# Kernel optimization log

Hardware: AMD Instinct MI355X
Metric: run time of the kernel (lower is better)

## Reference

```python
import jax, jax.numpy as jnp
import numpy as np

ALPHA = 0.2  # LeakyReLU negative slope
NEG_BIG = jnp.float32(-9e15)


def _leaky_relu(x):
    return jnp.where(x > 0, x, ALPHA * x)


def gat_layer(h, adj, w, a):
    """One GATLayer with concat=True (ELU output), dropout=0 (eval mode).
    h: [N, F_in], adj: [N, N] int, w: [F_in, F_out], a: [2*F_out, 1].
    """
    Wh = h @ w                         # [N, F_out]
    f_out = w.shape[1]
    Wh1 = Wh @ a[:f_out]               # [N, 1]
    Wh2 = Wh @ a[f_out:]               # [N, 1]
    e = _leaky_relu(Wh1 + Wh2.T)       # [N, N] dense additive scores
    att = jnp.where(adj > 0, e, NEG_BIG)
    att = jax.nn.softmax(att, axis=1)  # row softmax
    return jax.nn.elu(att @ Wh)        # [N, F_out]


def setup_inputs() -> dict:
    N, F_IN, H, NHEADS = 4096, 128, 64, 4
    key = jax.random.key(0)
    ks = jax.random.split(key, 9)
    s = jnp.float32(0.1)  # keep logits in a sane range
    x = jax.random.normal(ks[0], (N, F_IN), jnp.float32)
    adj = jax.random.randint(ks[1], (N, N), 0, 2, jnp.int32)
    return {
        "x": x,
        "adj": adj,
        "w_heads": jax.random.normal(ks[2], (NHEADS, F_IN, H), jnp.float32) * s,
        "a_heads": jax.random.normal(ks[3], (NHEADS, 2 * H, 1), jnp.float32) * s,
        "w_out": jax.random.normal(ks[4], (NHEADS * H, H), jnp.float32) * s,
        "a_out": jax.random.normal(ks[5], (2 * H, 1), jnp.float32) * s,
        "lin_w": jax.random.normal(ks[6], (H, F_IN), jnp.float32) * s,
        "lin_b": jnp.zeros((H,), jnp.float32),
        "outlin_w": jax.random.normal(ks[7], (H, H), jnp.float32) * s,
        "outlin_b": jnp.zeros((H,), jnp.float32),
    }


def reference(x, adj, w_heads, a_heads, w_out, a_out, lin_w, lin_b, outlin_w, outlin_b):
    N = x.shape[0]
    x_residual = x @ lin_w.T + lin_b                      # nn.Linear(input, hidden)
    # multi-head GAT layers, concatenated along features
    heads = jax.vmap(gat_layer, in_axes=(None, None, 0, 0))(x, adj, w_heads, a_heads)  # [nh, N, H]
    hcat = jnp.transpose(heads, (1, 0, 2)).reshape(N, -1)  # [N, nh*H]
    out = gat_layer(hcat, adj, w_out, a_out)               # out_att (concat=True => ELU)
    out = (x_residual + out) @ outlin_w.T + outlin_b       # out_linear
    return jax.nn.elu(out)
```

## Files before the change

kernel.cpp:

```cpp
#include <hip/hip_runtime.h>
#include <hip/hip_bf16.h>
#include <stdint.h>

#define F_IN 128
#define H 64
#define NH 4
#define KCH_H 8
#define KCH_O 16
#define LOG2E 1.44269504088896f

typedef __attribute__((ext_vector_type(8))) short bf16x8;
typedef __attribute__((ext_vector_type(4))) float floatx4;

static __device__ __forceinline__ unsigned short f2bf(float v) {
    __hip_bfloat16 b = __float2bfloat16(v);
    return *(unsigned short*)&b;
}

__global__ void prep_kernel(const int4* __restrict__ adj4,
                            unsigned char* __restrict__ adjp,
                            const float* __restrict__ x,
                            const float* __restrict__ w_heads,
                            const float* __restrict__ a_heads,
                            const float* __restrict__ lin_w,
                            const float* __restrict__ lin_b,
                            unsigned short* __restrict__ Bpk,
                            float* __restrict__ x_res,
                            float* __restrict__ s1h,
                            float* __restrict__ s2h, int N) {
    int bid = blockIdx.x;
    int tid = threadIdx.x;
    int KT = N >> 5;
    if (bid < 2 * N) {
        int row = bid >> 1;
        int c0 = ((bid & 1) * 256 + tid) * 8;
        const int4* p = adj4 + ((size_t)row * N + c0) / 4;
        int4 a = p[0], b = p[1];
        unsigned int byte =
            (unsigned)(a.x > 0) | ((unsigned)(a.y > 0) << 1) |
            ((unsigned)(a.z > 0) << 2) | ((unsigned)(a.w > 0) << 3) |
            ((unsigned)(b.x > 0) << 4) | ((unsigned)(b.y > 0) << 5) |
            ((unsigned)(b.z > 0) << 6) | ((unsigned)(b.w > 0) << 7);
        int kt = c0 >> 5, q = (c0 >> 3) & 3;
        adjp[((size_t)(row >> 4) * KT + kt) * 64 + q * 16 + (row & 15)] =
            (unsigned char)byte;
        return;
    }
    int blk = bid - 2 * N;
    int h = tid >> 6, f = tid & 63;
    int i0 = blk * 8;
    __shared__ float xs[8][F_IN];
    for (int e = tid; e < 8 * F_IN; e += 256)
        xs[e >> 7][e & 127] = x[(size_t)(i0 + (e >> 7)) * F_IN + (e & 127)];
    __syncthreads();
    float acc[8];
#pragma unroll
    for (int r = 0; r < 8; ++r) acc[r] = 0.f;
    float xr0 = 0.f, xr1 = 0.f;
    const float* w = w_heads + (size_t)h * F_IN * H + f;
    const float* lw = lin_w + (size_t)f * F_IN;
#pragma unroll 4
    for (int k = 0; k < F_IN; ++k) {
        float wv = w[(size_t)k * H];
#pragma unroll
        for (int r = 0; r < 8; ++r) acc[r] += xs[r][k] * wv;
        float wx = lw[k];
        xr0 += xs[h][k] * wx;
        xr1 += xs[h + 4][k] * wx;
    }
    {
        int kt = i0 >> 5, qq = (i0 >> 3) & 3;
        union { unsigned short s[8]; uint4 v; } t;
#pragma unroll
        for (int r = 0; r < 8; ++r) t.s[r] = f2bf(acc[r]);
        unsigned short* d = Bpk +
            (((size_t)(h * KT + kt) * 4 + (f >> 4)) * 64 + qq * 16 + (f & 15)) * 8;
        *(uint4*)d = t.v;
    }
    float b = lin_b[f];
    x_res[(size_t)(i0 + h) * H + f] = xr0 + b;
    x_res[(size_t)(i0 + h + 4) * H + f] = xr1 + b;
    float a1v = a_heads[(size_t)h * 2 * H + f];
    float a2v = a_heads[(size_t)h * 2 * H + H + f];
#pragma unroll
    for (int r = 0; r < 8; ++r) {
        float t1 = acc[r] * a1v;
        float t2 = acc[r] * a2v;
#pragma unroll
        for (int off = 32; off > 0; off >>= 1) {
            t1 += __shfl_xor(t1, off, 64);
            t2 += __shfl_xor(t2, off, 64);
        }
        if (f == 0) {
            s1h[(size_t)h * N + i0 + r] = t1 * LOG2E;
            s2h[(size_t)h * N + i0 + r] = t2 * LOG2E;
        }
    }
}

template <int KTC>
__global__ __launch_bounds__(256, 8)
void pv2_kernel(const unsigned char* __restrict__ adjp,
                const unsigned short* __restrict__ Bpk,
                const float* __restrict__ s1a,
                const float* __restrict__ s2a,
                float* __restrict__ outp, float* __restrict__ lp,
                int out_stride, int N) {
    const int h = blockIdx.y, z = blockIdx.z;
    const int KT = N >> 5;
    const int kt0 = z * KTC;
    const int tid = threadIdx.x;
    const int wave = tid >> 6, lane = tid & 63;
    const int n = lane & 15, q = lane >> 4;
    const int i0w = (blockIdx.x * 4 + wave) * 16;

    __shared__ float s2s[KTC * 32];
    __shared__ unsigned short ldsB[2][2048];

    const float4* s2src = (const float4*)(s2a + (size_t)h * N + kt0 * 32);
    for (int e = tid; e < KTC * 8; e += 256) ((float4*)s2s)[e] = s2src[e];

    const unsigned short* Bb = Bpk + ((size_t)h * KT + kt0) * 2048;
    uint4 breg = *(const uint4*)(Bb + tid * 8);
    *(uint4*)&ldsB[0][tid * 8] = breg;
    breg = *(const uint4*)(Bb + 2048 + tid * 8);

    const unsigned char* ap = adjp + ((size_t)(i0w >> 4) * KT + kt0) * 64 + lane;
    unsigned int a_c = ap[0];
    unsigned int a_n = ap[64];
    const float s1v = s1a[(size_t)h * N + i0w + n];

    floatx4 acc[4];
    floatx4 accl = {0.f, 0.f, 0.f, 0.f};
#pragma unroll
    for (int g = 0; g < 4; ++g) acc[g] = (floatx4){0.f, 0.f, 0.f, 0.f};

    bf16x8 ones;
    {
        short one = (n == 0) ? (short)0x3F80 : (short)0;
#pragma unroll
        for (int jj = 0; jj < 8; ++jj) ones[jj] = one;
    }

    __syncthreads();

#pragma unroll 2
    for (int k = 0; k < KTC; ++k) {
        if (k + 1 < KTC) *(uint4*)&ldsB[(k + 1) & 1][tid * 8] = breg;
        unsigned int a_2 = 0;
        if (k + 2 < KTC) {
            breg = *(const uint4*)(Bb + (size_t)(k + 2) * 2048 + tid * 8);
            a_2 = ap[(size_t)(k + 2) * 64];
        }

        float4 sa = *(const float4*)&s2s[k * 32 + q * 8];
        float4 sb = *(const float4*)&s2s[k * 32 + q * 8 + 4];
        const float* sv = (const float*)&sa;
        const float* sw = (const float*)&sb;
        float e[8];
#pragma unroll
        for (int jj = 0; jj < 8; ++jj) {
            float sj = (jj < 4 ? sv[jj] : sw[jj - 4]);
            float tt = s1v + sj;
            float lr = fmaxf(tt, 0.2f * tt);
            lr = (a_c & (1u << jj)) ? lr : -150.f;
            e[jj] = __builtin_amdgcn_exp2f(lr);
        }
        union { unsigned int u[4]; bf16x8 v; } u;
        u.u[0] = __builtin_amdgcn_perm(__float_as_uint(e[1]), __float_as_uint(e[0]), 0x07060302u);
        u.u[1] = __builtin_amdgcn_perm(__float_as_uint(e[3]), __float_as_uint(e[2]), 0x07060302u);
        u.u[2] = __builtin_amdgcn_perm(__float_as_uint(e[5]), __float_as_uint(e[4]), 0x07060302u);
        u.u[3] = __builtin_amdgcn_perm(__float_as_uint(e[7]), __float_as_uint(e[6]), 0x07060302u);

        bf16x8 bf0 = *(const bf16x8*)&ldsB[k & 1][0 * 512 + lane * 8];
        bf16x8 bf1 = *(const bf16x8*)&ldsB[k & 1][1 * 512 + lane * 8];
        bf16x8 bf2 = *(const bf16x8*)&ldsB[k & 1][2 * 512 + lane * 8];
        bf16x8 bf3 = *(const bf16x8*)&ldsB[k & 1][3 * 512 + lane * 8];

        acc[0] = __builtin_amdgcn_mfma_f32_16x16x32_bf16(u.v, bf0, acc[0], 0, 0, 0);
        acc[1] = __builtin_amdgcn_mfma_f32_16x16x32_bf16(u.v, bf1, acc[1], 0, 0, 0);
        acc[2] = __builtin_amdgcn_mfma_f32_16x16x32_bf16(u.v, bf2, acc[2], 0, 0, 0);
        acc[3] = __builtin_amdgcn_mfma_f32_16x16x32_bf16(u.v, bf3, acc[3], 0, 0, 0);
        accl   = __builtin_amdgcn_mfma_f32_16x16x32_bf16(u.v, ones, accl, 0, 0, 0);

        a_c = a_n;
        a_n = a_2;
        __syncthreads();
    }

    float* obase = outp + ((size_t)z * N + i0w) * out_stride + h * 64;
#pragma unroll
    for (int r = 0; r < 4; ++r) {
        int rr = q * 4 + r;
        float* op = obase + (size_t)rr * out_stride + n;
        op[0]  = acc[0][r];
        op[16] = acc[1][r];
        op[32] = acc[2][r];
        op[48] = acc[3][r];
    }
    if (n == 0) {
        float* lrow = lp + ((size_t)z * gridDim.y + h) * N + i0w;
#pragma unroll
        for (int r = 0; r < 4; ++r) lrow[q * 4 + r] = accl[r];
    }
}

__global__ void whout2_kernel(const float* __restrict__ hcp,
                              const float* __restrict__ lhp,
                              const float* __restrict__ w_out,
                              const float* __restrict__ a_out,
                              unsigned short* __restrict__ BpkO,
                              float* __restrict__ s1o,
                              float* __restrict__ s2o, int N) {
    int tid = threadIdx.x;
    int i0 = blockIdx.x * 8;
    int KT = N >> 5;
    __shared__ float hs[8][256];
    __shared__ float linv[8][NH];
    if (tid < 8 * NH) {
        int r = tid >> 2, hd = tid & 3;
        float l = 0.f;
#pragma unroll
        for (int p = 0; p < KCH_H; ++p)
            l += lhp[((size_t)p * NH + hd) * N + i0 + r];
        linv[r][hd] = 1.f / fmaxf(l, 1e-30f);
    }
    __syncthreads();
    const size_t ps = (size_t)N * 256;
    for (int e = tid; e < 8 * 256; e += 256) {
        int r = e >> 8, k = e & 255;
        size_t off = (size_t)(i0 + r) * 256 + k;
        float v = 0.f;
#pragma unroll
        for (int p = 0; p < KCH_H; ++p) v += hcp[p * ps + off];
        v *= linv[r][k >> 6];
        hs[r][k] = v > 0.f ? v : expm1f(v);
    }
    __syncthreads();
    int f = tid & 63, rl = tid >> 6;
    float a0 = 0.f, a1 = 0.f;
#pragma unroll 4
    for (int k = 0; k < 256; ++k) {
        float wv = w_out[(size_t)k * H + f];
        a0 += hs[rl][k] * wv;
        a1 += hs[rl + 4][k] * wv;
    }
    float w1 = a_out[f], w2 = a_out[H + f];
    float t10 = a0 * w1, t20 = a0 * w2, t11 = a1 * w1, t21 = a1 * w2;
#pragma unroll
    for (int off = 32; off > 0; off >>= 1) {
        t10 += __shfl_xor(t10, off, 64);
        t20 += __shfl_xor(t20, off, 64);
        t11 += __shfl_xor(t11, off, 64);
        t21 += __shfl_xor(t21, off, 64);
    }
    if (f == 0) {
        s1o[i0 + rl] = t10 * LOG2E;
        s2o[i0 + rl] = t20 * LOG2E;
        s1o[i0 + rl + 4] = t11 * LOG2E;
        s2o[i0 + rl + 4] = t21 * LOG2E;
    }
    __syncthreads();
    float* wsW = &hs[0][0];
    wsW[rl * 64 + f] = a0;
    wsW[(rl + 4) * 64 + f] = a1;
    __syncthreads();
    if (tid < 64) {
        int kt = i0 >> 5, qq = (i0 >> 3) & 3;
        int g = tid >> 4, nn = tid & 15;
        union { unsigned short s[8]; uint4 v; } t;
#pragma unroll
        for (int r = 0; r < 8; ++r) t.s[r] = f2bf(wsW[r * 64 + g * 16 + nn]);
        unsigned short* d = BpkO +
            (((size_t)kt * 4 + g) * 64 + qq * 16 + nn) * 8;
        *(uint4*)d = t.v;
    }
}

__global__ void final2_kernel(const float* __restrict__ o2p,
                              const float* __restrict__ lop,
                              const float* __restrict__ x_res,
                              const float* __restrict__ outlin_w,
                              const float* __restrict__ outlin_b,
                              float* __restrict__ out, int N) {
    int tid = threadIdx.x;
    int f = tid & 63, rl = tid >> 6;
    int i0 = blockIdx.x * 8;
    __shared__ float hs[8][H];
    __shared__ float linv[8];
    if (tid < 8) {
        float l = 0.f;
#pragma unroll
        for (int p = 0; p < KCH_O; ++p) l += lop[(size_t)p * N + i0 + tid];
        linv[tid] = 1.f / fmaxf(l, 1e-30f);
    }
    __syncthreads();
    const size_t ps = (size_t)N * 64;
    for (int e = tid; e < 8 * 64; e += 256) {
        int r = e >> 6, ff = e & 63;
        size_t off = (size_t)(i0 + r) * 64 + ff;
        float v = 0.f;
#pragma unroll
        for (int p = 0; p < KCH_O; ++p) v += o2p[p * ps + off];
        v *= linv[r];
        v = v > 0.f ? v : expm1f(v);
        hs[r][ff] = v + x_res[off];
    }
    __syncthreads();
    float b = outlin_b[f];
    float a0 = b, a1 = b;
#pragma unroll 8
    for (int k = 0; k < H; ++k) {
        float wv = outlin_w[(size_t)f * H + k];
        a0 += hs[rl][k] * wv;
        a1 += hs[rl + 4][k] * wv;
    }
    a0 = a0 > 0.f ? a0 : expm1f(a0);
    a1 = a1 > 0.f ? a1 : expm1f(a1);
    out[(size_t)(i0 + rl) * H + f] = a0;
    out[(size_t)(i0 + rl + 4) * H + f] = a1;
}

extern "C" void kernel_launch(void* const* d_in, const int* in_sizes, int n_in,
                              void* d_out, int out_size, void* d_ws, size_t ws_size,
                              hipStream_t stream) {
    const float* x        = (const float*)d_in[0];
    const int*   adj      = (const int*)d_in[1];
    const float* w_heads  = (const float*)d_in[2];
    const float* a_heads  = (const float*)d_in[3];
    const float* w_out    = (const float*)d_in[4];
    const float* a_out    = (const float*)d_in[5];
    const float* lin_w    = (const float*)d_in[6];
    const float* lin_b    = (const float*)d_in[7];
    const float* outlin_w = (const float*)d_in[8];
    const float* outlin_b = (const float*)d_in[9];
    float* out = (float*)d_out;

    const int N = in_sizes[0] / F_IN;
    const int KT = N >> 5;

    char* p = (char*)d_ws;
    float* part   = (float*)p;  p += (size_t)KCH_H * N * 256 * 4;
    float* x_res  = (float*)p;  p += (size_t)N * 64 * 4;
    float* s1h    = (float*)p;  p += (size_t)NH * N * 4;
    float* s2h    = (float*)p;  p += (size_t)NH * N * 4;
    float* s1o    = (float*)p;  p += (size_t)N * 4;
    float* s2o    = (float*)p;  p += (size_t)N * 4;
    float* lh_part = (float*)p; p += (size_t)KCH_H * NH * N * 4;
    float* lo_part = (float*)p; p += (size_t)KCH_O * N * 4;
    unsigned short* Bpk  = (unsigned short*)p;  p += (size_t)NH * KT * 2048 * 2;
    unsigned short* BpkO = (unsigned short*)p;  p += (size_t)KT * 2048 * 2;
    unsigned char* adjp  = (unsigned char*)p;   p += (size_t)(N / 16) * KT * 64;

    prep_kernel<<<2 * N + N / 8, 256, 0, stream>>>(
        (const int4*)adj, adjp, x, w_heads, a_heads, lin_w, lin_b,
        Bpk, x_res, s1h, s2h, N);
    pv2_kernel<16><<<dim3(N / 64, NH, KCH_H), 256, 0, stream>>>(
        adjp, Bpk, s1h, s2h, part, lh_part, NH * H, N);
    whout2_kernel<<<N / 8, 256, 0, stream>>>(part, lh_part, w_out, a_out,
                                             BpkO, s1o, s2o, N);
    pv2_kernel<8><<<dim3(N / 64, 1, KCH_O), 256, 0, stream>>>(
        adjp, BpkO, s1o, s2o, part, lo_part, H, N);
    final2_kernel<<<N / 8, 256, 0, stream>>>(part, lo_part, x_res, outlin_w, outlin_b, out, N);
}
```

Before: 228.4 us.

## Store split-K partial outputs in bf16 and split prep into adjacency-pack and projection kernels

The split-K partial attention outputs written by the PV kernel are now stored as bf16 instead of fp32, halving the write and read traffic of the partial buffers that the reduction kernels consume. The combined prep kernel is split into a dedicated adjacency bit-packing kernel, where each block handles 16 rows and loops over column tiles, and a separate projection kernel. Storing partials in bf16 loses precision before the split-K summation, and the extra launch adds overhead.

New measurement: 202.4 us. -11.4%, faster.

```diff
diff --git a/kernel.cpp b/kernel.cpp
--- a/kernel.cpp
+++ b/kernel.cpp
@@ -16,39 +16,49 @@
     __hip_bfloat16 b = __float2bfloat16(v);
     return *(unsigned short*)&b;
 }
-
-__global__ void prep_kernel(const int4* __restrict__ adj4,
-                            unsigned char* __restrict__ adjp,
-                            const float* __restrict__ x,
-                            const float* __restrict__ w_heads,
-                            const float* __restrict__ a_heads,
-                            const float* __restrict__ lin_w,
-                            const float* __restrict__ lin_b,
-                            unsigned short* __restrict__ Bpk,
-                            float* __restrict__ x_res,
-                            float* __restrict__ s1h,
-                            float* __restrict__ s2h, int N) {
-    int bid = blockIdx.x;
+static __device__ __forceinline__ float bf2f(unsigned short u) {
+    return __uint_as_float((unsigned int)u << 16);
+}
+
+__global__ void pack_adjp_kernel(const int* __restrict__ adj,
+                                 unsigned char* __restrict__ adjp,
+                                 int N, int KT) {
+    int it = blockIdx.x;
+    int half = blockIdx.y;
+    int i0 = it * 16;
     int tid = threadIdx.x;
-    int KT = N >> 5;
-    if (bid < 2 * N) {
-        int row = bid >> 1;
-        int c0 = ((bid & 1) * 256 + tid) * 8;
-        const int4* p = adj4 + ((size_t)row * N + c0) / 4;
-        int4 a = p[0], b = p[1];
-        unsigned int byte =
+    int n = tid & 15, q = (tid >> 4) & 3, w = tid >> 6;
+    const int* row = adj + (size_t)(i0 + n) * N;
+    unsigned char* dst = adjp + (size_t)it * KT * 64;
+    int ktbase = half * (KT / 2) + w;
+#pragma unroll 4
+    for (int j = 0; j < KT / 8; ++j) {
+        int kt = ktbase + 4 * j;
+        int c0 = kt * 32 + q * 8;
+        int4 a = *(const int4*)(row + c0);
+        int4 b = *(const int4*)(row + c0 + 4);
+        unsigned byte =
             (unsigned)(a.x > 0) | ((unsigned)(a.y > 0) << 1) |
             ((unsigned)(a.z > 0) << 2) | ((unsigned)(a.w > 0) << 3) |
             ((unsigned)(b.x > 0) << 4) | ((unsigned)(b.y > 0) << 5) |
             ((unsigned)(b.z > 0) << 6) | ((unsigned)(b.w > 0) << 7);
-        int kt = c0 >> 5, q = (c0 >> 3) & 3;
-        adjp[((size_t)(row >> 4) * KT + kt) * 64 + q * 16 + (row & 15)] =
-            (unsigned char)byte;
-        return;
-    }
-    int blk = bid - 2 * N;
+        dst[kt * 64 + q * 16 + n] = (unsigned char)byte;
+    }
+}
+
+__global__ void wh_fused_kernel(const float* __restrict__ x,
+                                const float* __restrict__ w_heads,
+                                const float* __restrict__ a_heads,
+                                const float* __restrict__ lin_w,
+                                const float* __restrict__ lin_b,
+                                unsigned short* __restrict__ Bpk,
+                                float* __restrict__ x_res,
+                                float* __restrict__ s1h,
+                                float* __restrict__ s2h, int N) {
+    int tid = threadIdx.x;
     int h = tid >> 6, f = tid & 63;
-    int i0 = blk * 8;
+    int i0 = blockIdx.x * 8;
+    int KT = N >> 5;
     __shared__ float xs[8][F_IN];
     for (int e = tid; e < 8 * F_IN; e += 256)
         xs[e >> 7][e & 127] = x[(size_t)(i0 + (e >> 7)) * F_IN + (e & 127)];
@@ -104,7 +114,7 @@
                 const unsigned short* __restrict__ Bpk,
                 const float* __restrict__ s1a,
                 const float* __restrict__ s2a,
-                float* __restrict__ outp, float* __restrict__ lp,
+                unsigned short* __restrict__ outp, float* __restrict__ lp,
                 int out_stride, int N) {
     const int h = blockIdx.y, z = blockIdx.z;
     const int KT = N >> 5;
@@ -188,15 +198,15 @@
         __syncthreads();
     }
 
-    float* obase = outp + ((size_t)z * N + i0w) * out_stride + h * 64;
+    unsigned short* obase = outp + ((size_t)z * N + i0w) * out_stride + h * 64;
 #pragma unroll
     for (int r = 0; r < 4; ++r) {
         int rr = q * 4 + r;
-        float* op = obase + (size_t)rr * out_stride + n;
-        op[0]  = acc[0][r];
-        op[16] = acc[1][r];
-        op[32] = acc[2][r];
-        op[48] = acc[3][r];
+        unsigned short* op = obase + (size_t)rr * out_stride + n;
+        op[0]  = f2bf(acc[0][r]);
+        op[16] = f2bf(acc[1][r]);
+        op[32] = f2bf(acc[2][r]);
+        op[48] = f2bf(acc[3][r]);
     }
     if (n == 0) {
         float* lrow = lp + ((size_t)z * gridDim.y + h) * N + i0w;
@@ -205,7 +215,7 @@
     }
 }
 
-__global__ void whout2_kernel(const float* __restrict__ hcp,
+__global__ void whout2_kernel(const unsigned short* __restrict__ hcp,
                               const float* __restrict__ lhp,
                               const float* __restrict__ w_out,
                               const float* __restrict__ a_out,
@@ -232,7 +242,7 @@
         size_t off = (size_t)(i0 + r) * 256 + k;
         float v = 0.f;
 #pragma unroll
-        for (int p = 0; p < KCH_H; ++p) v += hcp[p * ps + off];
+        for (int p = 0; p < KCH_H; ++p) v += bf2f(hcp[p * ps + off]);
         v *= linv[r][k >> 6];
         hs[r][k] = v > 0.f ? v : expm1f(v);
     }
@@ -277,7 +287,7 @@
     }
 }
 
-__global__ void final2_kernel(const float* __restrict__ o2p,
+__global__ void final2_kernel(const unsigned short* __restrict__ o2p,
                               const float* __restrict__ lop,
                               const float* __restrict__ x_res,
                               const float* __restrict__ outlin_w,
@@ -301,7 +311,7 @@
         size_t off = (size_t)(i0 + r) * 64 + ff;
         float v = 0.f;
 #pragma unroll
-        for (int p = 0; p < KCH_O; ++p) v += o2p[p * ps + off];
+        for (int p = 0; p < KCH_O; ++p) v += bf2f(o2p[p * ps + off]);
         v *= linv[r];
         v = v > 0.f ? v : expm1f(v);
         hs[r][ff] = v + x_res[off];
@@ -340,7 +350,7 @@
     const int KT = N >> 5;
 
     char* p = (char*)d_ws;
-    float* part   = (float*)p;  p += (size_t)KCH_H * N * 256 * 4;
+    unsigned short* part = (unsigned short*)p;  p += (size_t)KCH_H * N * 256 * 2;
     float* x_res  = (float*)p;  p += (size_t)N * 64 * 4;
     float* s1h    = (float*)p;  p += (size_t)NH * N * 4;
     float* s2h    = (float*)p;  p += (size_t)NH * N * 4;
@@ -352,9 +362,9 @@
     unsigned short* BpkO = (unsigned short*)p;  p += (size_t)KT * 2048 * 2;
     unsigned char* adjp  = (unsigned char*)p;   p += (size_t)(N / 16) * KT * 64;
 
-    prep_kernel<<<2 * N + N / 8, 256, 0, stream>>>(
-        (const int4*)adj, adjp, x, w_heads, a_heads, lin_w, lin_b,
-        Bpk, x_res, s1h, s2h, N);
+    pack_adjp_kernel<<<dim3(N / 16, 2), 256, 0, stream>>>(adj, adjp, N, KT);
+    wh_fused_kernel<<<N / 8, 256, 0, stream>>>(x, w_heads, a_heads, lin_w, lin_b,
+                                               Bpk, x_res, s1h, s2h, N);
     pv2_kernel<16><<<dim3(N / 64, NH, KCH_H), 256, 0, stream>>>(
         adjp, Bpk, s1h, s2h, part, lh_part, NH * H, N);
     whout2_kernel<<<N / 8, 256, 0, stream>>>(part, lh_part, w_out, a_out,
```
